# Kernel tuning notes

Hardware: AMD Instinct MI355X
Metric: run time of the kernel (lower is better)

## Reference

```python
import jax, jax.numpy as jnp
import numpy as np

N = 100_000      # nodes
E = 3_200_000    # directed edges
F_IN = 128       # node feature dim
H = 16           # hidden channels


def setup_inputs() -> dict:
    key = jax.random.key(0)
    k0, k1, k2, k3, k4, k5 = jax.random.split(key, 6)
    x = jax.random.normal(k0, (N, F_IN), dtype=jnp.float32)
    edge_index = jax.random.randint(k1, (2, E), 0, N, dtype=jnp.int32)
    W1 = jax.random.normal(k2, (F_IN, H), dtype=jnp.float32) * (1.0 / np.sqrt(F_IN))
    b1 = jax.random.normal(k3, (H,), dtype=jnp.float32) * 0.02
    W2 = jax.random.normal(k4, (H, 1), dtype=jnp.float32) * (1.0 / np.sqrt(H))
    b2 = jax.random.normal(k5, (1,), dtype=jnp.float32) * 0.02
    return {"x": x, "edge_index": edge_index, "W1": W1, "b1": b1, "W2": W2, "b2": b2}


def _gcn_conv(x, src, dst, deg_inv_sqrt, W, b):
    # PyG GCNConv: h = x @ W; out_i = sum_{j->i} norm_ij * h_j + b
    # norm_ij = deg_i^-1/2 * deg_j^-1/2 (degrees include self-loops)
    n = x.shape[0]
    h = x @ W                                   # [N, out]
    norm = deg_inv_sqrt[src] * deg_inv_sqrt[dst]  # [E+N]
    msg = h[src] * norm[:, None]                # gather + scale
    out = jax.ops.segment_sum(msg, dst, num_segments=n)
    return out + b


def reference(x, edge_index, W1, b1, W2, b2):
    n = x.shape[0]
    loops = jnp.arange(n, dtype=edge_index.dtype)
    src = jnp.concatenate([edge_index[0], loops])  # self-loops appended
    dst = jnp.concatenate([edge_index[1], loops])
    # degree of destination nodes (with self-loops), shared by both layers
    deg = jax.ops.segment_sum(jnp.ones_like(dst, dtype=x.dtype), dst, num_segments=n)
    deg_inv_sqrt = jax.lax.rsqrt(jnp.maximum(deg, 1.0))  # deg >= 1 due to self-loops

    h = jax.nn.relu(_gcn_conv(x, src, dst, deg_inv_sqrt, W1, b1))
    out = _gcn_conv(h, src, dst, deg_inv_sqrt, W2, b2)
    return out
```

## Files before the change

### kernel.cpp

```cpp
#include <hip/hip_runtime.h>
#include <hip/hip_fp16.h>

#define FIN 128
#define HC 16
#define NB 391
#define NSL 391
#define BKT 256
#define CELL 64
#define STRIDE 80
#define ESLICE 8188

typedef _Float16 half8 __attribute__((ext_vector_type(8)));
typedef float f32x4 __attribute__((ext_vector_type(4)));

__global__ __launch_bounds__(1024) void scatter_kernel(const int* __restrict__ src,
                                                       const int* __restrict__ dst,
                                                       unsigned int* __restrict__ ebuf,
                                                       unsigned char* __restrict__ cntcell, int E) {
    __shared__ int cur[NB];
    int blk = blockIdx.x, t = threadIdx.x;
    for (int i = t; i < NB; i += 1024) cur[i] = 0;
    __syncthreads();
    int s = blk * ESLICE, e = min(E, s + ESLICE);
    int boff = blk * CELL;
    if (s < e) {
        int n4 = (e - s) >> 2;
        const int4* d4 = (const int4*)(dst + s);
        const int4* s4 = (const int4*)(src + s);
        for (int i = t; i < n4; i += 1024) {
            int4 dd = d4[i];
            int4 ss = s4[i];
            int b0 = dd.x >> 8, p0 = atomicAdd(&cur[b0], 1);
            ebuf[(size_t)b0 * (NSL * CELL) + boff + p0] = ((unsigned)ss.x << 8) | (unsigned)(dd.x & 255);
            int b1 = dd.y >> 8, p1 = atomicAdd(&cur[b1], 1);
            ebuf[(size_t)b1 * (NSL * CELL) + boff + p1] = ((unsigned)ss.y << 8) | (unsigned)(dd.y & 255);
            int b2 = dd.z >> 8, p2 = atomicAdd(&cur[b2], 1);
            ebuf[(size_t)b2 * (NSL * CELL) + boff + p2] = ((unsigned)ss.z << 8) | (unsigned)(dd.z & 255);
            int b3 = dd.w >> 8, p3 = atomicAdd(&cur[b3], 1);
            ebuf[(size_t)b3 * (NSL * CELL) + boff + p3] = ((unsigned)ss.w << 8) | (unsigned)(dd.w & 255);
        }
    }
    __syncthreads();
    for (int i = t; i < NB; i += 1024) cntcell[(size_t)blk * NB + i] = (unsigned char)cur[i];
}

__global__ __launch_bounds__(1024) void sortdis_h1_kernel(
    const unsigned int* __restrict__ ebuf, const unsigned char* __restrict__ cntcell,
    const float* __restrict__ x, const float* __restrict__ W1,
    int* __restrict__ csr, int* __restrict__ deg, float* __restrict__ dis,
    __half* __restrict__ hs16, int n) {
    __shared__ int cnt[BKT];
    __shared__ unsigned char cc[NB];
    __shared__ float disL[BKT];
    int b = blockIdx.x, t = threadIdx.x;
    if (t < BKT) cnt[t] = 0;
    for (int i = t; i < NB; i += 1024) cc[i] = cntcell[(size_t)i * NB + b];
    __syncthreads();
    int wave = t >> 6, lane = t & 63;
    size_t cbase = (size_t)b * BKT * STRIDE;
    size_t ebase = (size_t)b * (NSL * CELL);
    for (int c = wave; c < NSL; c += 16) {
        int m = cc[c];
        if (lane < m) {
            unsigned u = ebuf[ebase + (size_t)c * CELL + lane];
            int l = u & 255;
            int r = atomicAdd(&cnt[l], 1);
            csr[cbase + l * STRIDE + r] = (int)(u >> 8);
        }
    }
    __syncthreads();
    if (t < BKT) {
        int node = b * BKT + t;
        float dv = rsqrtf((float)cnt[t] + 1.0f);
        disL[t] = dv;
        if (node < n) {
            deg[node] = cnt[t];
            dis[node] = dv;
        }
    }
    __syncthreads();
    int r = lane & 15, g = lane >> 4;
    half8 bfrag[4];
#pragma unroll
    for (int i = 0; i < 4; ++i)
#pragma unroll
        for (int j = 0; j < 8; ++j)
            bfrag[i][j] = (_Float16)W1[(i * 32 + g * 8 + j) * HC + r];
    int lrow = wave * 16;
    int grow = b * BKT + lrow + r;
    const f32x4* xr = (const f32x4*)(x + (size_t)(grow < n ? grow : n - 1) * FIN);
    f32x4 v[8];
#pragma unroll
    for (int i = 0; i < 4; ++i) {
        int idx = i * 8 + g * 2;
        v[2 * i] = xr[idx];
        v[2 * i + 1] = xr[idx + 1];
    }
    f32x4 acc = {0.f, 0.f, 0.f, 0.f};
#pragma unroll
    for (int i = 0; i < 4; ++i) {
        half8 afrag;
        afrag[0] = (_Float16)v[2 * i][0]; afrag[1] = (_Float16)v[2 * i][1];
        afrag[2] = (_Float16)v[2 * i][2]; afrag[3] = (_Float16)v[2 * i][3];
        afrag[4] = (_Float16)v[2 * i + 1][0]; afrag[5] = (_Float16)v[2 * i + 1][1];
        afrag[6] = (_Float16)v[2 * i + 1][2]; afrag[7] = (_Float16)v[2 * i + 1][3];
        acc = __builtin_amdgcn_mfma_f32_16x16x32_f16(afrag, bfrag[i], acc, 0, 0, 0);
    }
#pragma unroll
    for (int j = 0; j < 4; ++j) {
        int lr = lrow + g * 4 + j;
        int orow = b * BKT + lr;
        if (orow < n) hs16[(size_t)orow * HC + r] = __float2half(acc[j] * disL[lr]);
    }
}

#define GSTEP4(T, SIDX, MM, A01, A23)                                       \
    {                                                                       \
        int e_ = (T) * 16 + eg;                                             \
        int s_ = __shfl((SIDX), e_);                                        \
        uint2 raw_ = *(const uint2*)(hs16 + (size_t)s_ * 16 + cp4 * 4);     \
        float2 f01_ = __half22float2(*(__half2*)&raw_.x);                   \
        float2 f23_ = __half22float2(*(__half2*)&raw_.y);                   \
        if (e_ < (MM)) {                                                    \
            (A01).x += f01_.x; (A01).y += f01_.y;                           \
            (A23).x += f23_.x; (A23).y += f23_.y;                           \
        }                                                                   \
    }

__global__ void pull_layer1_kernel(const int* __restrict__ deg, const int* __restrict__ csr,
                                   const __half* __restrict__ hs16,
                                   const float* __restrict__ b1, const float* __restrict__ W2,
                                   float* __restrict__ h2s, int n) {
    int wid = (blockIdx.x * blockDim.x + threadIdx.x) >> 6;
    int n0 = wid * 2;
    if (n0 >= n) return;
    int n1 = n0 + 1;
    int lane = threadIdx.x & 63;
    int cp4 = lane & 3;
    int eg = lane >> 2;
    int p0 = csr[n0 * STRIDE + lane];
    int p1 = csr[n1 * STRIDE + lane];
    int2 mpair = ((const int2*)deg)[wid];
    int m0 = mpair.x, m1 = mpair.y;
    int c0 = (lane < m0) ? p0 : 0;
    int c1 = (lane < m1) ? p1 : 0;
    int mm0 = min(m0, 64), mm1 = min(m1, 64);
    float2 a010 = {0.f, 0.f}, a230 = {0.f, 0.f};
    float2 a011 = {0.f, 0.f}, a231 = {0.f, 0.f};
    GSTEP4(0, c0, mm0, a010, a230) GSTEP4(0, c1, mm1, a011, a231)
    GSTEP4(1, c0, mm0, a010, a230) GSTEP4(1, c1, mm1, a011, a231)
    if (mm0 > 32) {
        GSTEP4(2, c0, mm0, a010, a230) GSTEP4(3, c0, mm0, a010, a230)
        for (int k = 64 + eg; k < m0; k += 16) {
            int s_ = csr[n0 * STRIDE + k];
            uint2 raw_ = *(const uint2*)(hs16 + (size_t)s_ * 16 + cp4 * 4);
            float2 f01_ = __half22float2(*(__half2*)&raw_.x);
            float2 f23_ = __half22float2(*(__half2*)&raw_.y);
            a010.x += f01_.x; a010.y += f01_.y; a230.x += f23_.x; a230.y += f23_.y;
        }
    }
    if (mm1 > 32) {
        GSTEP4(2, c1, mm1, a011, a231) GSTEP4(3, c1, mm1, a011, a231)
        for (int k = 64 + eg; k < m1; k += 16) {
            int s_ = csr[n1 * STRIDE + k];
            uint2 raw_ = *(const uint2*)(hs16 + (size_t)s_ * 16 + cp4 * 4);
            float2 f01_ = __half22float2(*(__half2*)&raw_.x);
            float2 f23_ = __half22float2(*(__half2*)&raw_.y);
            a011.x += f01_.x; a011.y += f01_.y; a231.x += f23_.x; a231.y += f23_.y;
        }
    }
#pragma unroll
    for (int off = 4; off < 64; off <<= 1) {
        a010.x += __shfl_xor(a010.x, off); a010.y += __shfl_xor(a010.y, off);
        a230.x += __shfl_xor(a230.x, off); a230.y += __shfl_xor(a230.y, off);
        a011.x += __shfl_xor(a011.x, off); a011.y += __shfl_xor(a011.y, off);
        a231.x += __shfl_xor(a231.x, off); a231.y += __shfl_xor(a231.y, off);
    }
    float4 bv = ((const float4*)b1)[cp4];
    float4 wv = ((const float4*)W2)[cp4];
    uint2 sr0 = *(const uint2*)(hs16 + (size_t)n0 * 16 + cp4 * 4);
    uint2 sr1 = *(const uint2*)(hs16 + (size_t)n1 * 16 + cp4 * 4);
    float2 s001 = __half22float2(*(__half2*)&sr0.x);
    float2 s023 = __half22float2(*(__half2*)&sr0.y);
    float2 s101 = __half22float2(*(__half2*)&sr1.x);
    float2 s123 = __half22float2(*(__half2*)&sr1.y);
    float d0 = rsqrtf((float)m0 + 1.0f);
    float d1 = rsqrtf((float)m1 + 1.0f);
    float v0 = fmaxf(fmaf(d0, a010.x + s001.x, bv.x), 0.f) * wv.x
             + fmaxf(fmaf(d0, a010.y + s001.y, bv.y), 0.f) * wv.y
             + fmaxf(fmaf(d0, a230.x + s023.x, bv.z), 0.f) * wv.z
             + fmaxf(fmaf(d0, a230.y + s023.y, bv.w), 0.f) * wv.w;
    float v1 = fmaxf(fmaf(d1, a011.x + s101.x, bv.x), 0.f) * wv.x
             + fmaxf(fmaf(d1, a011.y + s101.y, bv.y), 0.f) * wv.y
             + fmaxf(fmaf(d1, a231.x + s123.x, bv.z), 0.f) * wv.z
             + fmaxf(fmaf(d1, a231.y + s123.y, bv.w), 0.f) * wv.w;
    v0 += __shfl_xor(v0, 1); v1 += __shfl_xor(v1, 1);
    v0 += __shfl_xor(v0, 2); v1 += __shfl_xor(v1, 2);
    if (lane == 0) {
        h2s[n0] = v0 * d0;
        h2s[n1] = v1 * d1;
    }
}

__global__ void pull_layer2_kernel(const int* __restrict__ deg, const int* __restrict__ csr,
                                   const float* __restrict__ h2s,
                                   const float* __restrict__ b2, float* __restrict__ out, int n) {
    int g = blockIdx.x * blockDim.x + threadIdx.x;
    int node = g >> 4;
    if (node >= n) return;
    int q = g & 15;
    int start = node * STRIDE;
    int m = deg[node];
    float a = 0.f;
    int k = q;
    for (; k + 16 < m; k += 32) {
        int i0 = csr[start + k];
        int i1 = csr[start + k + 16];
        a += h2s[i0] + h2s[i1];
    }
    for (; k < m; k += 16) a += h2s[csr[start + k]];
    a += __shfl_xor(a, 1);
    a += __shfl_xor(a, 2);
    a += __shfl_xor(a, 4);
    a += __shfl_xor(a, 8);
    if (q == 0) out[node] = rsqrtf((float)m + 1.0f) * (a + h2s[node]) + b2[0];
}

extern "C" void kernel_launch(void* const* d_in, const int* in_sizes, int n_in,
                              void* d_out, int out_size, void* d_ws, size_t ws_size,
                              hipStream_t stream) {
    const float* x  = (const float*)d_in[0];
    const int* ei   = (const int*)d_in[1];
    const float* W1 = (const float*)d_in[2];
    const float* b1 = (const float*)d_in[3];
    const float* W2 = (const float*)d_in[4];
    const float* b2 = (const float*)d_in[5];
    float* out = (float*)d_out;

    const int n = in_sizes[0] / FIN;
    const int E = in_sizes[1] / 2;
    const int* src = ei;
    const int* dst = ei + E;

    const size_t EB = (size_t)NB * NSL * CELL;
    unsigned int* ebuf  = (unsigned int*)d_ws;
    int* csr            = (int*)(ebuf + EB);
    unsigned char* cc   = (unsigned char*)(csr + (size_t)100000 * STRIDE + 128);
    int* deg            = (int*)(cc + 152888);
    float* dis          = (float*)(deg + n);
    float* h2s          = dis + n;
    __half* hs16        = (__half*)(h2s + n);

    scatter_kernel<<<NSL, 1024, 0, stream>>>(src, dst, ebuf, cc, E);
    sortdis_h1_kernel<<<NB, 1024, 0, stream>>>(ebuf, cc, x, W1, csr, deg, dis, hs16, n);
    pull_layer1_kernel<<<(n / 2 * 64 + 511) / 512, 512, 0, stream>>>(deg, csr, hs16, b1, W2, h2s, n);
    pull_layer2_kernel<<<(n * 16 + 511) / 512, 512, 0, stream>>>(deg, csr, h2s, b2, out, n);
}
```

Before: 107.6 us.

## Split x@W1 MFMA out of sort kernel into separate LDS-staged kernel

Moves the dense x@W1 projection out of the bucket-sort/degree kernel into its own kernel with 64-row tiles, 256 threads and coalesced float4 loads of x staged through shared memory. The aim is to read the 51 MB x tensor with more blocks and better coalescing than the 391-block sort kernel, where each lane loaded scattered row segments. The cost is an extra kernel launch and re-reading dis from global memory.

```diff
diff --git a/kernel.cpp b/kernel.cpp
--- a/kernel.cpp
+++ b/kernel.cpp
@@ -44,14 +44,12 @@
     for (int i = t; i < NB; i += 1024) cntcell[(size_t)blk * NB + i] = (unsigned char)cur[i];
 }
 
-__global__ __launch_bounds__(1024) void sortdis_h1_kernel(
-    const unsigned int* __restrict__ ebuf, const unsigned char* __restrict__ cntcell,
-    const float* __restrict__ x, const float* __restrict__ W1,
-    int* __restrict__ csr, int* __restrict__ deg, float* __restrict__ dis,
-    __half* __restrict__ hs16, int n) {
+__global__ __launch_bounds__(1024) void sortdis_kernel(const unsigned int* __restrict__ ebuf,
+                                                       const unsigned char* __restrict__ cntcell,
+                                                       int* __restrict__ csr, int* __restrict__ deg,
+                                                       float* __restrict__ dis, int n) {
     __shared__ int cnt[BKT];
     __shared__ unsigned char cc[NB];
-    __shared__ float disL[BKT];
     int b = blockIdx.x, t = threadIdx.x;
     if (t < BKT) cnt[t] = 0;
     for (int i = t; i < NB; i += 1024) cc[i] = cntcell[(size_t)i * NB + b];
@@ -71,46 +69,58 @@
     __syncthreads();
     if (t < BKT) {
         int node = b * BKT + t;
-        float dv = rsqrtf((float)cnt[t] + 1.0f);
-        disL[t] = dv;
         if (node < n) {
             deg[node] = cnt[t];
-            dis[node] = dv;
-        }
-    }
-    __syncthreads();
+            dis[node] = rsqrtf((float)cnt[t] + 1.0f);
+        }
+    }
+}
+
+__global__ void h1_mfma_kernel(const float* __restrict__ x, const float* __restrict__ W1,
+                               const float* __restrict__ dis, __half* __restrict__ hs16, int n) {
+    __shared__ float xs[64][132];
+    int t = threadIdx.x;
+    int wave = t >> 6;
+    int lane = t & 63;
     int r = lane & 15, g = lane >> 4;
+    int rowbase0 = blockIdx.x * 64;
+#pragma unroll
+    for (int it = 0; it < 8; ++it) {
+        int i = it * 256 + t;
+        int row = i >> 5, c4 = i & 31;
+        int grow = rowbase0 + row;
+        const float4* xr = (const float4*)(x + (size_t)(grow < n ? grow : n - 1) * FIN);
+        float4 v = xr[c4];
+        xs[row][c4 * 4 + 0] = v.x;
+        xs[row][c4 * 4 + 1] = v.y;
+        xs[row][c4 * 4 + 2] = v.z;
+        xs[row][c4 * 4 + 3] = v.w;
+    }
     half8 bfrag[4];
 #pragma unroll
     for (int i = 0; i < 4; ++i)
 #pragma unroll
         for (int j = 0; j < 8; ++j)
             bfrag[i][j] = (_Float16)W1[(i * 32 + g * 8 + j) * HC + r];
-    int lrow = wave * 16;
-    int grow = b * BKT + lrow + r;
-    const f32x4* xr = (const f32x4*)(x + (size_t)(grow < n ? grow : n - 1) * FIN);
-    f32x4 v[8];
+    __syncthreads();
+    int rowbase = wave * 16;
+    f32x4 acc = {0.f, 0.f, 0.f, 0.f};
 #pragma unroll
     for (int i = 0; i < 4; ++i) {
-        int idx = i * 8 + g * 2;
-        v[2 * i] = xr[idx];
-        v[2 * i + 1] = xr[idx + 1];
-    }
-    f32x4 acc = {0.f, 0.f, 0.f, 0.f};
-#pragma unroll
-    for (int i = 0; i < 4; ++i) {
+        const float4* rowp = (const float4*)&xs[rowbase + r][i * 32 + g * 8];
+        float4 v0 = rowp[0];
+        float4 v1 = rowp[1];
         half8 afrag;
-        afrag[0] = (_Float16)v[2 * i][0]; afrag[1] = (_Float16)v[2 * i][1];
-        afrag[2] = (_Float16)v[2 * i][2]; afrag[3] = (_Float16)v[2 * i][3];
-        afrag[4] = (_Float16)v[2 * i + 1][0]; afrag[5] = (_Float16)v[2 * i + 1][1];
-        afrag[6] = (_Float16)v[2 * i + 1][2]; afrag[7] = (_Float16)v[2 * i + 1][3];
+        afrag[0] = (_Float16)v0.x; afrag[1] = (_Float16)v0.y;
+        afrag[2] = (_Float16)v0.z; afrag[3] = (_Float16)v0.w;
+        afrag[4] = (_Float16)v1.x; afrag[5] = (_Float16)v1.y;
+        afrag[6] = (_Float16)v1.z; afrag[7] = (_Float16)v1.w;
         acc = __builtin_amdgcn_mfma_f32_16x16x32_f16(afrag, bfrag[i], acc, 0, 0, 0);
     }
 #pragma unroll
     for (int j = 0; j < 4; ++j) {
-        int lr = lrow + g * 4 + j;
-        int orow = b * BKT + lr;
-        if (orow < n) hs16[(size_t)orow * HC + r] = __float2half(acc[j] * disL[lr]);
+        int orow = rowbase0 + rowbase + g * 4 + j;
+        if (orow < n) hs16[(size_t)orow * HC + r] = __float2half(acc[j] * dis[orow]);
     }
 }
 
@@ -252,7 +262,8 @@
     __half* hs16        = (__half*)(h2s + n);
 
     scatter_kernel<<<NSL, 1024, 0, stream>>>(src, dst, ebuf, cc, E);
-    sortdis_h1_kernel<<<NB, 1024, 0, stream>>>(ebuf, cc, x, W1, csr, deg, dis, hs16, n);
+    sortdis_kernel<<<NB, 1024, 0, stream>>>(ebuf, cc, csr, deg, dis, n);
+    h1_mfma_kernel<<<(n + 63) / 64, 256, 0, stream>>>(x, W1, dis, hs16, n);
     pull_layer1_kernel<<<(n / 2 * 64 + 511) / 512, 512, 0, stream>>>(deg, csr, hs16, b1, W2, h2s, n);
     pull_layer2_kernel<<<(n * 16 + 511) / 512, 512, 0, stream>>>(deg, csr, h2s, b2, out, n);
 }
```

Result: no change. 109.1 us (+1.4%).
